# Optimization experiments

Measured on AMD Instinct MI355X. Metric: run time of the kernel, lower is better.

Reference implementation:

```python
import jax, jax.numpy as jnp
import numpy as np
import math

CTX_LEN = 2048
N_EMB = 256
HEAD_SIZE = 256
N_HEADS = 8
HEAD_DIM = HEAD_SIZE // N_HEADS  # 32
B, T = 4, 2048


def setup_inputs() -> dict:
    key = jax.random.key(0)
    k1, k2, k3, k4 = jax.random.split(key, 4)
    x = jax.random.normal(k1, (B, T, N_EMB), dtype=jnp.float32)
    # torch Linear(n_emb, 3*head_size, bias=False): store as [in, out] for x @ W
    w_attn = jax.random.normal(k2, (N_EMB, 3 * HEAD_SIZE), dtype=jnp.float32) * 0.02
    pos_embs = jax.random.normal(k3, (N_HEADS, CTX_LEN, HEAD_DIM), dtype=jnp.float32) * 0.02
    w_proj = jax.random.normal(k4, (HEAD_SIZE, N_EMB), dtype=jnp.float32) * 0.02
    b_proj = jnp.zeros((N_EMB,), dtype=jnp.float32)
    return {"x": x, "w_attn": w_attn, "pos_embs": pos_embs,
            "w_proj": w_proj, "b_proj": b_proj}


def reference(x, w_attn, pos_embs, w_proj, b_proj):
    Bsz, Tlen, _ = x.shape
    qkv = x @ w_attn                               # [B,T,3*HS]
    K, Q, V = jnp.split(qkv, 3, axis=-1)           # split order: K, Q, V (as in source)
    def heads(t):                                  # [B,T,HS] -> [B,H,T,hd]
        return t.reshape(Bsz, Tlen, N_HEADS, HEAD_DIM).transpose(0, 2, 1, 3)
    K, Q, V = heads(K), heads(Q), heads(V)

    # relative position term with skew trick
    pe = pos_embs[:, -Tlen:, :]                    # [H,T,hd]
    S_rel = jnp.einsum('bhtd,hsd->bhts', Q, pe)    # [B,H,T,T]
    flip_mask = jnp.flip(jnp.tril(jnp.ones((Tlen, Tlen), dtype=x.dtype)), axis=1)
    S_rel = S_rel * flip_mask
    # pad a zero column at the front, reshape [T+1,T], drop first row -> skew
    S_rel = jnp.pad(S_rel, ((0, 0), (0, 0), (0, 0), (1, 0)))
    S_rel = S_rel.reshape(Bsz, N_HEADS, Tlen + 1, Tlen)[:, :, 1:, :]

    scores = (jnp.einsum('bhtd,bhsd->bhts', Q, K) + S_rel) / math.sqrt(HEAD_DIM)
    causal = jnp.where(jnp.tril(jnp.ones((Tlen, Tlen), dtype=bool)), 0.0, -1e9).astype(x.dtype)
    scores = scores + causal
    attn = jax.nn.softmax(scores, axis=-1)         # dropout omitted (eval mode)

    out = jnp.einsum('bhts,bhsd->bhtd', attn, V)   # [B,H,T,hd]
    out = out.transpose(0, 2, 1, 3).reshape(Bsz, Tlen, HEAD_SIZE)
    return out @ w_proj + b_proj
```

## Files before the change

### kernel.cpp

```cpp
#include <hip/hip_runtime.h>
#include <math.h>

#define BB 4
#define TT 2048
#define TTP 2176
#define NEMB 256
#define NH 8
#define HD 32

typedef __attribute__((ext_vector_type(8))) short bf8;
typedef __attribute__((ext_vector_type(4))) float f4;

static __device__ __forceinline__ unsigned short f2bf(float f) {
    union { float f; unsigned u; } v; v.f = f;
    unsigned r = v.u + 0x7FFF + ((v.u >> 16) & 1);
    return (unsigned short)(r >> 16);
}
static __device__ __forceinline__ float bf2f(unsigned short s) {
    union { unsigned u; float f; } v; v.u = ((unsigned)s) << 16;
    return v.f;
}

template <int CTRL>
static __device__ __forceinline__ float dppmv(float x) {
    return __int_as_float(__builtin_amdgcn_mov_dpp(__float_as_int(x), CTRL, 0xF, 0xF, true));
}
static __device__ __forceinline__ float rowsum16(float x) {
    x += dppmv<0xB1>(x);
    x += dppmv<0x4E>(x);
    x += dppmv<0x124>(x);
    x += dppmv<0x128>(x);
    return x;
}

static __device__ __forceinline__ void tcvt_body(const float* __restrict__ src,
                                                 unsigned short* __restrict__ dst,
                                                 int R, int C, int gx, int gy,
                                                 float (*t)[65], int tid) {
    const int c0 = gx * 64, r0 = gy * 64;
    #pragma unroll
    for (int p = 0; p < 4; ++p) {
        const int i = tid + p * 256;
        const int r = i >> 4, c4 = (i & 15) * 4;
        const float4 v = *(const float4*)(src + (long)(r0 + r) * C + c0 + c4);
        t[r][c4] = v.x; t[r][c4+1] = v.y; t[r][c4+2] = v.z; t[r][c4+3] = v.w;
    }
    __syncthreads();
    #pragma unroll
    for (int p = 0; p < 4; ++p) {
        const int i = tid + p * 256;
        const int cr = i >> 4, r4 = (i & 15) * 4;
        ushort4 vv;
        vv.x = f2bf(t[r4+0][cr]); vv.y = f2bf(t[r4+1][cr]);
        vv.z = f2bf(t[r4+2][cr]); vv.w = f2bf(t[r4+3][cr]);
        *(ushort4*)(dst + (long)(c0 + cr) * R + r0 + r4) = vv;
    }
}

__global__ __launch_bounds__(256) void prep(const float* __restrict__ pe,
                                            unsigned short* __restrict__ peb,
                                            const float* __restrict__ wa,
                                            unsigned short* __restrict__ waT,
                                            const float* __restrict__ wp,
                                            unsigned short* __restrict__ wpT) {
    __shared__ float t[64][65];
    const int bx = blockIdx.x, tid = threadIdx.x;
    if (bx < 544) {
        const int idx4 = bx * 256 + tid;
        const int h   = idx4 / 17408;
        const int rem = idx4 - h * 17408;
        const int u   = rem >> 3;
        const int d4  = (rem & 7) * 4;
        ushort4 o = make_ushort4(0, 0, 0, 0);
        if (u < TT) {
            const float4 v = *(const float4*)(pe + ((long)(h * TT + u)) * HD + d4);
            o.x = f2bf(v.x); o.y = f2bf(v.y); o.z = f2bf(v.z); o.w = f2bf(v.w);
        }
        *(ushort4*)(peb + ((long)(h * TTP + u)) * HD + d4) = o;
    } else if (bx < 592) {
        const int lo = bx - 544;
        tcvt_body(wa, waT, 256, 768, lo % 12, lo / 12, t, tid);
    } else {
        const int lo = bx - 592;
        tcvt_body(wp, wpT, 256, 256, lo % 4, lo / 4, t, tid);
    }
}

__global__ __launch_bounds__(256) void qkv_mfma(const float* __restrict__ xg,
                                                const unsigned short* __restrict__ Bg,
                                                unsigned short* __restrict__ Kb,
                                                unsigned short* __restrict__ Qb,
                                                unsigned short* __restrict__ Vt) {
    __shared__ unsigned short sm[13824];
    unsigned short* As = sm;
    unsigned short* Bs = sm + 9216;
    const int tid = threadIdx.x;
    const int wv = tid >> 6, L = tid & 63;
    const int l15 = L & 15, q = L >> 4;
    const int n0 = blockIdx.x * 64;
    const int m0 = blockIdx.y * 128;

    f4 acc[2][4];
    #pragma unroll
    for (int mt = 0; mt < 2; ++mt)
        #pragma unroll
        for (int nt = 0; nt < 4; ++nt) acc[mt][nt] = (f4){0.f,0.f,0.f,0.f};

    for (int kc = 0; kc < 4; ++kc) {
        const int k0 = kc * 64;
        __syncthreads();
        #pragma unroll
        for (int p = 0; p < 4; ++p) {
            const int i = tid + p * 256;
            const int r = i >> 3, c = i & 7;
            const float4 va = *(const float4*)(xg + (long)(m0 + r) * 256 + k0 + c * 8);
            const float4 vb = *(const float4*)(xg + (long)(m0 + r) * 256 + k0 + c * 8 + 4);
            ushort4 lo, hi;
            lo.x = f2bf(va.x); lo.y = f2bf(va.y); lo.z = f2bf(va.z); lo.w = f2bf(va.w);
            hi.x = f2bf(vb.x); hi.y = f2bf(vb.y); hi.z = f2bf(vb.z); hi.w = f2bf(vb.w);
            *(ushort4*)(As + r * 72 + c * 8)     = lo;
            *(ushort4*)(As + r * 72 + c * 8 + 4) = hi;
        }
        #pragma unroll
        for (int p = 0; p < 2; ++p) {
            const int i = tid + p * 256;
            const int r = i >> 3, c = i & 7;
            *(bf8*)(Bs + r * 72 + c * 8) = *(const bf8*)(Bg + (long)(n0 + r) * 256 + k0 + c * 8);
        }
        __syncthreads();
        #pragma unroll
        for (int kk = 0; kk < 2; ++kk) {
            const bf8 a0 = *(const bf8*)(As + (wv * 32 + l15) * 72 + kk * 32 + q * 8);
            const bf8 a1 = *(const bf8*)(As + (wv * 32 + 16 + l15) * 72 + kk * 32 + q * 8);
            #pragma unroll
            for (int nt = 0; nt < 4; ++nt) {
                const bf8 bb = *(const bf8*)(Bs + (nt * 16 + l15) * 72 + kk * 32 + q * 8);
                acc[0][nt] = __builtin_amdgcn_mfma_f32_16x16x32_bf16(a0, bb, acc[0][nt], 0, 0, 0);
                acc[1][nt] = __builtin_amdgcn_mfma_f32_16x16x32_bf16(a1, bb, acc[1][nt], 0, 0, 0);
            }
        }
    }

    const int sec = n0 >> 8;
    if (sec == 2) {
        unsigned short* Vs = sm;
        __syncthreads();
        #pragma unroll
        for (int mt = 0; mt < 2; ++mt) {
            const int sb = (wv >> 1) * 64;
            const int jb = 16 * q + ((2 * wv + mt) & 3);
            #pragma unroll
            for (int nt = 0; nt < 4; ++nt) {
                const int nl = nt * 16 + l15;
                const f4 a = acc[mt][nt];
                #pragma unroll
                for (int r = 0; r < 4; ++r)
                    Vs[nl * 132 + sb + jb + 4 * r] = f2bf(a[r]);
            }
        }
        __syncthreads();
        const int bloc = m0 >> 11;
        #pragma unroll
        for (int p = 0; p < 8; ++p) {
            const int gid = tid + p * 256;
            const int nl = gid >> 5;
            const int cg = (gid & 31) * 4;
            const int h  = ((n0 - 512) >> 5) + (nl >> 5);
            const long bh = (long)bloc * NH + h;
            *(ushort4*)(Vt + (bh * HD + (nl & 31)) * TT + (m0 & 2047) + cg) =
                *(ushort4*)(Vs + nl * 132 + cg);
        }
        return;
    }
    #pragma unroll
    for (int mt = 0; mt < 2; ++mt) {
        const int gm = m0 + wv * 32 + mt * 16 + q * 4;
        const int b = gm >> 11, tb = gm & 2047;
        #pragma unroll
        for (int nt = 0; nt < 4; ++nt) {
            const int gn = n0 + nt * 16 + l15;
            const int cc = gn & 255, h = cc >> 5, d = cc & 31;
            const long bh = (long)b * NH + h;
            const f4 a = acc[mt][nt];
            if (sec == 1) {
                #pragma unroll
                for (int r = 0; r < 4; ++r)
                    Qb[(bh * TT + tb + r) * HD + d] = f2bf(a[r] * 0.25506655788696527f);
            } else {
                #pragma unroll
                for (int r = 0; r < 4; ++r)
                    Kb[(bh * TT + tb + r) * HD + d] = f2bf(a[r]);
            }
        }
    }
}

__global__ __launch_bounds__(256) void attn_kernel(const unsigned short* __restrict__ Kb,
                                                   const unsigned short* __restrict__ Qb,
                                                   const unsigned short* __restrict__ Vtg,
                                                   const unsigned short* __restrict__ peb,
                                                   unsigned short* __restrict__ po,
                                                   float* __restrict__ pl) {
    __shared__ unsigned short lds[17152];
    unsigned short* Ks  = lds;
    unsigned short* PEs = lds + 2560;
    unsigned short* Vts = lds + 10240;
    unsigned short* Psw = lds + 12544 + (threadIdx.x >> 6) * 1152;

    const int tid = threadIdx.x;
    const int wv  = tid >> 6;
    const int L   = tid & 63;
    const int l15 = L & 15;
    const int q   = L >> 4;
    const int pair = blockIdx.x >> 1;
    const int sblk = blockIdx.x & 1;
    const int h = blockIdx.y, b = blockIdx.z;
    const long bh = (long)b * NH + h;
    const unsigned short* Kg = Kb  + bh * TT * HD;
    const unsigned short* Qg = Qb  + bh * TT * HD;
    const unsigned short* Vg = Vtg + bh * HD * TT;
    const unsigned short* Pg = peb + (long)h * TTP * HD;

    const int krow = tid >> 2, kc = tid & 3;
    const int vrow = tid >> 3, vc = tid & 7;
    const f4 z4 = {0.f, 0.f, 0.f, 0.f};
    const f4 m4 = {-16.f, -16.f, -16.f, -16.f};

    int saddr[4]; unsigned psel[4];
    #pragma unroll
    for (int r = 0; r < 4; ++r) {
        const int tcol = l15 + 15 - 4 * q - r;
        saddr[r] = ((q << 4) | (tcol & 15)) << 2;
        psel[r]  = (tcol < 16) ? 0x01000C0Cu : 0x03020C0Cu;
    }

    for (int half = 0; half < 2; ++half) {
        const int itile = half ? 15 - pair : pair;
        const int t0 = itile * 128;

        bf8 aq[2];
        #pragma unroll
        for (int mf = 0; mf < 2; ++mf)
            aq[mf] = *(const bf8*)(Qg + (t0 + wv * 32 + mf * 16 + l15) * HD + q * 8);
        f4 o[2][2];
        o[0][0] = z4; o[0][1] = z4; o[1][0] = z4; o[1][1] = z4;
        float l_st[2][4] = {{0.f,0.f,0.f,0.f},{0.f,0.f,0.f,0.f}};

        const int jtmax = 2 * itile + 1;
        for (int jt = sblk; jt <= jtmax; jt += 2) {
            const int s0 = jt * 64;
            const int ub0 = TT - 128 - t0 + s0;
            __syncthreads();
            *(bf8*)(Ks  + krow * 40 + kc * 8) = *(const bf8*)(Kg + (s0 + krow) * HD + kc * 8);
            *(bf8*)(Vts + vrow * 72 + vc * 8) = *(const bf8*)(Vg + vrow * TT + s0 + vc * 8);
            #pragma unroll
            for (int kk = 0; kk < 3; ++kk) {
                const int i  = tid + kk * 256;
                const int pr = i >> 2, pc = i & 3;
                *(bf8*)(PEs + pr * 40 + pc * 8) = *(const bf8*)(Pg + (long)(ub0 + pr) * HD + pc * 8);
            }
            __syncthreads();

            bf8 bk[4], bva[2], bvb[2];
            #pragma unroll
            for (int nt = 0; nt < 4; ++nt)
                bk[nt] = *(const bf8*)(Ks + (nt * 16 + l15) * 40 + q * 8);
            #pragma unroll
            for (int ks = 0; ks < 2; ++ks) {
                bva[ks] = *(const bf8*)(Vts + l15 * 72 + ks * 32 + q * 8);
                bvb[ks] = *(const bf8*)(Vts + (16 + l15) * 72 + ks * 32 + q * 8);
            }

            #pragma unroll
            for (int mf = 0; mf < 2; ++mf) {
                f4 sa[4], ra[5];
                #pragma unroll
                for (int nt = 0; nt < 4; ++nt)
                    sa[nt] = __builtin_amdgcn_mfma_f32_16x16x32_bf16(aq[mf], bk[nt], m4, 0, 0, 0);
                const int pebs = 112 - wv * 32 - mf * 16;
                #pragma unroll
                for (int nt = 0; nt < 5; ++nt) {
                    const bf8 bp = *(const bf8*)(PEs + (pebs + nt * 16 + l15) * 40 + q * 8);
                    ra[nt] = __builtin_amdgcn_mfma_f32_16x16x32_bf16(aq[mf], bp, z4, 0, 0, 0);
                }

                #pragma unroll
                for (int nb = 0; nb < 4; ++nb) {
                    #pragma unroll
                    for (int r = 0; r < 4; ++r) {
                        const unsigned packed = __builtin_amdgcn_perm(
                            (unsigned)__float_as_int(ra[nb + 1][r]),
                            (unsigned)__float_as_int(ra[nb][r]), 0x07060302u);
                        const int v = __builtin_amdgcn_ds_bpermute(saddr[r], (int)packed);
                        const unsigned sel = __builtin_amdgcn_perm((unsigned)v, (unsigned)v, psel[r]);
                        sa[nb][r] += __int_as_float((int)sel);
                    }
                }

                if (s0 + 63 > t0 + wv * 32 + mf * 16) {
                    #pragma unroll
                    for (int nb = 0; nb < 4; ++nb)
                        #pragma unroll
                        for (int r = 0; r < 4; ++r) {
                            const int s_l = s0 + nb * 16 + l15;
                            const int t_l = t0 + wv * 32 + mf * 16 + 4 * q + r;
                            if (s_l > t_l) sa[nb][r] = -1e30f;
                        }
                }

                #pragma unroll
                for (int r = 0; r < 4; ++r) {
                    const float p0 = exp2f(sa[0][r]);
                    const float p1 = exp2f(sa[1][r]);
                    const float p2 = exp2f(sa[2][r]);
                    const float p3 = exp2f(sa[3][r]);
                    l_st[mf][r] += (p0 + p1) + (p2 + p3);
                    const unsigned a0 = (unsigned)__float_as_int(p0) + 0x8000u;
                    const unsigned a1 = (unsigned)__float_as_int(p1) + 0x8000u;
                    const unsigned a2 = (unsigned)__float_as_int(p2) + 0x8000u;
                    const unsigned a3 = (unsigned)__float_as_int(p3) + 0x8000u;
                    uint2 w;
                    w.x = __builtin_amdgcn_perm(a1, a0, 0x07060302u);
                    w.y = __builtin_amdgcn_perm(a3, a2, 0x07060302u);
                    *(uint2*)(Psw + (4 * q + r) * 72 + 4 * l15) = w;
                }

                #pragma unroll
                for (int ks = 0; ks < 2; ++ks) {
                    const bf8 ap = *(const bf8*)(Psw + l15 * 72 + ks * 32 + q * 8);
                    o[mf][0] = __builtin_amdgcn_mfma_f32_16x16x32_bf16(ap, bva[ks], o[mf][0], 0, 0, 0);
                    o[mf][1] = __builtin_amdgcn_mfma_f32_16x16x32_bf16(ap, bvb[ks], o[mf][1], 0, 0, 0);
                }
            }
        }

        const long pt = (bh * 16 + itile) * 2 + sblk;
        unsigned short* pob = po + pt * 4096;
        #pragma unroll
        for (int mf = 0; mf < 2; ++mf)
            #pragma unroll
            for (int r = 0; r < 4; ++r) {
                const int row = wv * 32 + mf * 16 + 4 * q + r;
                pob[row * 32 + l15]      = f2bf(o[mf][0][r]);
                pob[row * 32 + 16 + l15] = f2bf(o[mf][1][r]);
                const float ls = rowsum16(l_st[mf][r]);
                if (l15 == 0) pl[pt * 128 + row] = ls;
            }
    }
}

__global__ __launch_bounds__(256) void proj_mfma(const unsigned short* __restrict__ po,
                                                 const float* __restrict__ pl,
                                                 const unsigned short* __restrict__ Bg,
                                                 const float* __restrict__ bias,
                                                 float* __restrict__ out) {
    __shared__ unsigned short sm[13824];
    unsigned short* As = sm;
    unsigned short* Bs = sm + 9216;
    const int tid = threadIdx.x;
    const int wv = tid >> 6, L = tid & 63;
    const int l15 = L & 15, q = L >> 4;
    const int n0 = blockIdx.x * 64;
    const int m0 = blockIdx.y * 128;

    f4 acc[2][4];
    #pragma unroll
    for (int mt = 0; mt < 2; ++mt)
        #pragma unroll
        for (int nt = 0; nt < 4; ++nt) acc[mt][nt] = (f4){0.f,0.f,0.f,0.f};

    for (int kc = 0; kc < 4; ++kc) {
        const int k0 = kc * 64;
        __syncthreads();
        #pragma unroll
        for (int p = 0; p < 4; ++p) {
            const int i = tid + p * 256;
            const int r = i >> 3, c = i & 7;
            const int gm = m0 + r;
            const int bloc = gm >> 11, t = gm & 2047;
            const int k = k0 + c * 8;
            const int hh = k >> 5, d0 = k & 31;
            const int tile = t >> 7, row = t & 127;
            const long pt0 = ((long)(bloc * NH + hh) * 16 + tile) * 2;
            const float l0 = pl[pt0 * 128 + row];
            const float l1 = pl[pt0 * 128 + 128 + row];
            const float inv = 1.0f / (l0 + l1);
            const unsigned short* p0 = po + pt0 * 4096 + row * 32 + d0;
            const unsigned short* p1 = p0 + 4096;
            const ushort4 a0 = *(const ushort4*)p0;
            const ushort4 a1 = *(const ushort4*)(p0 + 4);
            const ushort4 c0 = *(const ushort4*)p1;
            const ushort4 c1 = *(const ushort4*)(p1 + 4);
            ushort4 o0, o1;
            o0.x = f2bf((bf2f(a0.x) + bf2f(c0.x)) * inv);
            o0.y = f2bf((bf2f(a0.y) + bf2f(c0.y)) * inv);
            o0.z = f2bf((bf2f(a0.z) + bf2f(c0.z)) * inv);
            o0.w = f2bf((bf2f(a0.w) + bf2f(c0.w)) * inv);
            o1.x = f2bf((bf2f(a1.x) + bf2f(c1.x)) * inv);
            o1.y = f2bf((bf2f(a1.y) + bf2f(c1.y)) * inv);
            o1.z = f2bf((bf2f(a1.z) + bf2f(c1.z)) * inv);
            o1.w = f2bf((bf2f(a1.w) + bf2f(c1.w)) * inv);
            *(ushort4*)(As + r * 72 + c * 8)     = o0;
            *(ushort4*)(As + r * 72 + c * 8 + 4) = o1;
        }
        #pragma unroll
        for (int p = 0; p < 2; ++p) {
            const int i = tid + p * 256;
            const int r = i >> 3, c = i & 7;
            *(bf8*)(Bs + r * 72 + c * 8) = *(const bf8*)(Bg + (long)(n0 + r) * 256 + k0 + c * 8);
        }
        __syncthreads();
        #pragma unroll
        for (int kk = 0; kk < 2; ++kk) {
            const bf8 a0 = *(const bf8*)(As + (wv * 32 + l15) * 72 + kk * 32 + q * 8);
            const bf8 a1 = *(const bf8*)(As + (wv * 32 + 16 + l15) * 72 + kk * 32 + q * 8);
            #pragma unroll
            for (int nt = 0; nt < 4; ++nt) {
                const bf8 bb = *(const bf8*)(Bs + (nt * 16 + l15) * 72 + kk * 32 + q * 8);
                acc[0][nt] = __builtin_amdgcn_mfma_f32_16x16x32_bf16(a0, bb, acc[0][nt], 0, 0, 0);
                acc[1][nt] = __builtin_amdgcn_mfma_f32_16x16x32_bf16(a1, bb, acc[1][nt], 0, 0, 0);
            }
        }
    }

    #pragma unroll
    for (int mt = 0; mt < 2; ++mt) {
        const int gm = m0 + wv * 32 + mt * 16 + q * 4;
        #pragma unroll
        for (int nt = 0; nt < 4; ++nt) {
            const int gn = n0 + nt * 16 + l15;
            const float bv = bias[gn];
            #pragma unroll
            for (int r = 0; r < 4; ++r)
                out[(long)(gm + r) * NEMB + gn] = acc[mt][nt][r] + bv;
        }
    }
}

extern "C" void kernel_launch(void* const* d_in, const int* in_sizes, int n_in,
                              void* d_out, int out_size, void* d_ws, size_t ws_size,
                              hipStream_t stream) {
    const float* x      = (const float*)d_in[0];
    const float* w_attn = (const float*)d_in[1];
    const float* pe     = (const float*)d_in[2];
    const float* w_proj = (const float*)d_in[3];
    const float* b_proj = (const float*)d_in[4];
    float* out = (float*)d_out;

    char* base = (char*)d_ws;
    unsigned short* Kb   = (unsigned short*)(base);
    unsigned short* Qb   = (unsigned short*)(base + ( 4u << 20));
    unsigned short* Vt   = (unsigned short*)(base + ( 8u << 20));
    unsigned short* peb  = (unsigned short*)(base + (12u << 20));
    unsigned short* waT  = (unsigned short*)(base + (14u << 20));
    unsigned short* wpT  = (unsigned short*)(base + (29u << 19));
    unsigned short* po   = (unsigned short*)(base + (15u << 20));
    float*          pl   = (float*)        (base + (23u << 20));

    prep<<<dim3(608), 256, 0, stream>>>(pe, peb, w_attn, waT, w_proj, wpT);
    qkv_mfma<<<dim3(12, 64), 256, 0, stream>>>(x, waT, Kb, Qb, Vt);
    attn_kernel<<<dim3(16, NH, BB), 256, 0, stream>>>(Kb, Qb, Vt, peb, po, pl);
    proj_mfma<<<dim3(4, 64), 256, 0, stream>>>(po, pl, wpT, b_proj, out);
}
```

Before: 158.1 us.

## Stage Q/K epilogue through LDS for coalesced stores; share PE fragment loads

The QKV GEMM epilogue for Q and K now writes the accumulator tile into shared memory, then issues coalesced 8-byte vector stores to global memory. This replaces the scattered 2-byte stores. In the attention kernel, the positional-embedding B fragments are loaded once per tile into six registers and shared by both mf iterations, cutting LDS reads from ten to six. The cost is extra barriers and LDS traffic in the epilogue, plus higher register pressure in the attention loop.

```diff
diff --git a/kernel.cpp b/kernel.cpp
--- a/kernel.cpp
+++ b/kernel.cpp
@@ -172,25 +172,35 @@
         }
         return;
     }
-    #pragma unroll
-    for (int mt = 0; mt < 2; ++mt) {
-        const int gm = m0 + wv * 32 + mt * 16 + q * 4;
-        const int b = gm >> 11, tb = gm & 2047;
-        #pragma unroll
-        for (int nt = 0; nt < 4; ++nt) {
-            const int gn = n0 + nt * 16 + l15;
-            const int cc = gn & 255, h = cc >> 5, d = cc & 31;
-            const long bh = (long)b * NH + h;
-            const f4 a = acc[mt][nt];
-            if (sec == 1) {
+    {
+        unsigned short* Ts = sm;
+        const float qsc = (sec == 1) ? 0.25506655788696527f : 1.0f;
+        __syncthreads();
+        #pragma unroll
+        for (int mt = 0; mt < 2; ++mt) {
+            const int tl0 = wv * 32 + mt * 16 + q * 4;
+            #pragma unroll
+            for (int nt = 0; nt < 4; ++nt) {
+                const int nl = nt * 16 + l15;
+                const f4 a = acc[mt][nt];
                 #pragma unroll
                 for (int r = 0; r < 4; ++r)
-                    Qb[(bh * TT + tb + r) * HD + d] = f2bf(a[r] * 0.25506655788696527f);
-            } else {
-                #pragma unroll
-                for (int r = 0; r < 4; ++r)
-                    Kb[(bh * TT + tb + r) * HD + d] = f2bf(a[r]);
-            }
+                    Ts[(tl0 + r) * 68 + nl] = f2bf(a[r] * qsc);
+            }
+        }
+        __syncthreads();
+        const int bloc = m0 >> 11;
+        unsigned short* dst = (sec == 1) ? Qb : Kb;
+        #pragma unroll
+        for (int p = 0; p < 8; ++p) {
+            const int gid = tid + p * 256;
+            const int tl = gid >> 4;
+            const int c4 = (gid & 15) * 4;
+            const int h  = ((n0 & 255) >> 5) + (c4 >> 5);
+            const int d  = c4 & 31;
+            const long bh = (long)bloc * NH + h;
+            const int t = (m0 & 2047) + tl;
+            *(ushort4*)(dst + (bh * TT + t) * HD + d) = *(ushort4*)(Ts + tl * 68 + c4);
         }
     }
 }
@@ -261,7 +271,7 @@
             }
             __syncthreads();
 
-            bf8 bk[4], bva[2], bvb[2];
+            bf8 bk[4], bva[2], bvb[2], bp[6];
             #pragma unroll
             for (int nt = 0; nt < 4; ++nt)
                 bk[nt] = *(const bf8*)(Ks + (nt * 16 + l15) * 40 + q * 8);
@@ -270,6 +280,10 @@
                 bva[ks] = *(const bf8*)(Vts + l15 * 72 + ks * 32 + q * 8);
                 bvb[ks] = *(const bf8*)(Vts + (16 + l15) * 72 + ks * 32 + q * 8);
             }
+            const int pebs1 = 96 - wv * 32;
+            #pragma unroll
+            for (int j = 0; j < 6; ++j)
+                bp[j] = *(const bf8*)(PEs + (pebs1 + j * 16 + l15) * 40 + q * 8);
 
             #pragma unroll
             for (int mf = 0; mf < 2; ++mf) {
@@ -277,12 +291,9 @@
                 #pragma unroll
                 for (int nt = 0; nt < 4; ++nt)
                     sa[nt] = __builtin_amdgcn_mfma_f32_16x16x32_bf16(aq[mf], bk[nt], m4, 0, 0, 0);
-                const int pebs = 112 - wv * 32 - mf * 16;
-                #pragma unroll
-                for (int nt = 0; nt < 5; ++nt) {
-                    const bf8 bp = *(const bf8*)(PEs + (pebs + nt * 16 + l15) * 40 + q * 8);
-                    ra[nt] = __builtin_amdgcn_mfma_f32_16x16x32_bf16(aq[mf], bp, z4, 0, 0, 0);
-                }
+                #pragma unroll
+                for (int nt = 0; nt < 5; ++nt)
+                    ra[nt] = __builtin_amdgcn_mfma_f32_16x16x32_bf16(aq[mf], bp[nt + 1 - mf], z4, 0, 0, 0);
 
                 #pragma unroll
                 for (int nb = 0; nb < 4; ++nb) {
```

Measured after the change: 157.2 us. Within noise of the previous version (-0.6%).
